# Kernel optimization log

Hardware: AMD Instinct MI355X
Metric: run time of the kernel (lower is better)

## Reference

```python
import jax, jax.numpy as jnp
import numpy as np

N, E, D, H, OUT = 100000, 1600000, 64, 64, 4


def _glorot(key, i, o):
    s = (6.0 / (i + o)) ** 0.5
    return jax.random.uniform(key, (i, o), jnp.float32, -s, s)


def setup_inputs() -> dict:
    key = jax.random.key(0)
    ks = jax.random.split(key, 5)
    x = jax.random.normal(ks[0], (N, D), jnp.float32)
    edge_index = jax.random.randint(ks[1], (2, E), 0, N, jnp.int32)
    return {
        "x": x,
        "edge_index": edge_index,
        "W0": _glorot(ks[2], D, H), "b0": jnp.zeros((H,), jnp.float32),
        "W1": _glorot(ks[3], H, H), "b1": jnp.zeros((H,), jnp.float32),
        "W2": _glorot(ks[4], H, OUT), "b2": jnp.zeros((OUT,), jnp.float32),
    }


def _gcn_layer(x, src, dst, W, b):
    # WeightedGCNConv.forward: remove_self_loops, then gcn_norm with
    # add_self_loops=True (self-loop weight 1), symmetric normalization,
    # scatter-add aggregation, then Linear.
    n = x.shape[0]
    w = (src != dst).astype(x.dtype)           # zero out original self loops
    deg = jax.ops.segment_sum(w, dst, num_segments=n) + 1.0  # +1 from added self loop
    dis = jax.lax.rsqrt(deg)                   # deg >= 1, no inf
    norm = dis[src] * w * dis[dst]             # [E]
    agg = jax.ops.segment_sum(norm[:, None] * x[src], dst, num_segments=n)
    agg = agg + (dis * dis)[:, None] * x       # self-loop contribution
    return agg @ W + b


def reference(x, edge_index, W0, b0, W1, b1, W2, b2):
    src, dst = edge_index[0], edge_index[1]    # flow source_to_target
    # Dropout is identity in eval mode.
    h = jax.nn.relu(_gcn_layer(x, src, dst, W0, b0))
    h = jax.nn.relu(_gcn_layer(h, src, dst, W1, b1))
    return _gcn_layer(h, src, dst, W2, b2)     # [N, 4]
```

## Files before the change

### kernel.cpp

```cpp
#include <hip/hip_runtime.h>
#include <hip/hip_fp16.h>


#define BLK 256
#define NBITS 7
#define NBW   (1 << NBITS)
#define G     8
#define CHUNK 4096
#define EPT   (CHUNK / BLK)
#define CAPG  384
#define PAD   16

__global__ void k_zero_i(int* __restrict__ p, int n) {
    int i = blockIdx.x * blockDim.x + threadIdx.x;
    if (i < n) p[i] = 0;
}

__global__ void k_binA(const int* __restrict__ src, const int* __restrict__ dst,
                       int* __restrict__ bcur, int* __restrict__ binned,
                       int E, int nb) {
    __shared__ int lcnt[1024];
    __shared__ int lbase[1024];
    int t = threadIdx.x;
    int g = blockIdx.x & (G - 1);
    for (int i = t; i < nb; i += BLK) lcnt[i] = 0;
    __syncthreads();

    int e0 = blockIdx.x * CHUNK;
    int bs[EPT], vs[EPT];
#pragma unroll
    for (int i = 0; i < EPT; ++i) {
        int e = e0 + i * BLK + t;
        bs[i] = -1;
        if (e < E) {
            int s = src[e], d = dst[e];
            if (s != d) {
                bs[i] = d >> NBITS;
                vs[i] = (s << NBITS) | (d & (NBW - 1));
                atomicAdd(&lcnt[bs[i]], 1);
            }
        }
    }
    __syncthreads();
    for (int i = t; i < nb; i += BLK) {
        int c = lcnt[i];
        lbase[i] = c ? atomicAdd(&bcur[(g * nb + i) * PAD], c) : 0;
    }
    __syncthreads();
    for (int i = t; i < nb; i += BLK) lcnt[i] = 0;
    __syncthreads();
#pragma unroll
    for (int i = 0; i < EPT; ++i) {
        if (bs[i] >= 0) {
            int p = lbase[bs[i]] + atomicAdd(&lcnt[bs[i]], 1);
            if (p < CAPG) binned[(size_t)(g * nb + bs[i]) * CAPG + p] = vs[i];
        }
    }
}

__global__ void k_bscan(const int* __restrict__ bcur, int* __restrict__ bbase, int nb) {
    __shared__ int sh[1024];
    int t = threadIdx.x;
    int v = 0;
    if (t < nb)
        for (int g = 0; g < G; ++g) v += min(bcur[(g * nb + t) * PAD], CAPG);
    sh[t] = v;
    __syncthreads();
    for (int off = 1; off < 1024; off <<= 1) {
        int u = (t >= off) ? sh[t - off] : 0;
        __syncthreads();
        sh[t] += u;
        __syncthreads();
    }
    if (t < nb) bbase[t] = sh[t] - v;
}

__global__ void k_binB(const int* __restrict__ bcur, const int* __restrict__ binned,
                       const int* __restrict__ bbase, int* __restrict__ rowstart,
                       float* __restrict__ dis, int* __restrict__ srcs,
                       int n, int nb) {
    __shared__ int cnt[NBW];
    __shared__ int scan[NBW];
    int b = blockIdx.x;
    int t = threadIdx.x;
    if (t < NBW) cnt[t] = 0;
    __syncthreads();
    for (int g = 0; g < G; ++g) {
        int m = min(bcur[(g * nb + b) * PAD], CAPG);
        const int* reg = binned + (size_t)(g * nb + b) * CAPG;
        for (int i = t; i < m; i += BLK)
            atomicAdd(&cnt[reg[i] & (NBW - 1)], 1);
    }
    __syncthreads();
    int c = 0;
    if (t < NBW) { c = cnt[t]; scan[t] = c; }
    __syncthreads();
    for (int off = 1; off < NBW; off <<= 1) {
        int u = (t < NBW && t >= off) ? scan[t - off] : 0;
        __syncthreads();
        if (t < NBW) scan[t] += u;
        __syncthreads();
    }
    int base = bbase[b];
    if (t < NBW) {
        int excl = scan[t] - c;
        int node = b * NBW + t;
        if (node < n) {
            rowstart[node] = base + excl;
            dis[node] = rsqrtf((float)c + 1.0f);
        }
        if (node == n) rowstart[n] = base + excl;
    }
    __syncthreads();
    if (t < NBW) scan[t] = scan[t] - c;
    __syncthreads();
    for (int g = 0; g < G; ++g) {
        int m = min(bcur[(g * nb + b) * PAD], CAPG);
        const int* reg = binned + (size_t)(g * nb + b) * CAPG;
        for (int i = t; i < m; i += BLK) {
            int v = reg[i];
            int p = atomicAdd(&scan[v & (NBW - 1)], 1);
            srcs[base + p] = v >> NBITS;
        }
    }
}

__device__ __forceinline__ float ldf(const float* p, long i) { return p[i]; }
__device__ __forceinline__ float ldf(const __half* p, long i) { return __half2float(p[i]); }

template <bool RELU, typename TIN>
__global__ void k_gemm64(const TIN* __restrict__ in, const float* __restrict__ W,
                         const float* __restrict__ dis, __half* __restrict__ z16, int n) {
    __shared__ float rows[4][64];
    int c  = threadIdx.x & 63;
    int r4 = threadIdx.x >> 6;
    float Wr[64];
#pragma unroll
    for (int k = 0; k < 64; ++k) Wr[k] = W[k * 64 + c];
    const float4* rp = reinterpret_cast<const float4*>(&rows[r4][0]);
    for (long base = (long)blockIdx.x * 4; base < n; base += (long)gridDim.x * 4) {
        long row = base + r4;
        __syncthreads();
        if (row < n) {
            float v = ldf(in, row * 64 + c);
            rows[r4][c] = RELU ? fmaxf(v, 0.0f) : v;
        }
        __syncthreads();
        if (row < n) {
            float acc = 0.0f;
#pragma unroll
            for (int k4 = 0; k4 < 16; ++k4) {
                float4 rv = rp[k4];
                acc = fmaf(rv.x, Wr[4 * k4 + 0], acc);
                acc = fmaf(rv.y, Wr[4 * k4 + 1], acc);
                acc = fmaf(rv.z, Wr[4 * k4 + 2], acc);
                acc = fmaf(rv.w, Wr[4 * k4 + 3], acc);
            }
            z16[row * 64 + c] = __float2half(dis[row] * acc);
        }
    }
}

__global__ void k_gemm4(const __half* __restrict__ in, const float* __restrict__ W,
                        const float* __restrict__ dis, float* __restrict__ z2, int n) {
    __shared__ float Wl[64 * 4];
    if (threadIdx.x < 64 * 4) Wl[threadIdx.x] = W[threadIdx.x];
    __syncthreads();
    long idx = (long)blockIdx.x * blockDim.x + threadIdx.x;
    long row = idx >> 2;
    int c    = (int)(idx & 3);
    if (row < n) {
        float acc = 0.0f;
#pragma unroll
        for (int k = 0; k < 64; ++k)
            acc = fmaf(fmaxf(__half2float(in[row * 64 + k]), 0.0f), Wl[k * 4 + c], acc);
        z2[idx] = dis[row] * acc;
    }
}

__global__ void k_aggregate(const __half2* __restrict__ z16, const int* __restrict__ rowstart,
                            const int* __restrict__ srcs, const float* __restrict__ dis,
                            const float* __restrict__ b, __half2* __restrict__ agg, int n) {
    int lane = threadIdx.x & 63;
    int node = blockIdx.x * (BLK / 64) + (threadIdx.x >> 6);
    if (node >= n) return;
    int p  = lane & 31;
    int hi = lane >> 5;
    float2 acc = make_float2(0.0f, 0.0f);
    if (hi == 0) {
        float2 v = __half22float2(z16[(long)node * 32 + p]);
        acc.x = v.x; acc.y = v.y;
    }
    int beg = rowstart[node], end = rowstart[node + 1];
    for (int base = beg; base < end; base += 64) {
        int rem = end - base;
        int m   = (rem < 64) ? rem : 64;
        int s   = (lane < m) ? srcs[base + lane] : 0;
        int me  = m & ~1;
#pragma unroll 8
        for (int j = 0; j < me; j += 2) {
            int sj = __shfl(s, j + hi);
            float2 v = __half22float2(z16[(long)sj * 32 + p]);
            acc.x += v.x; acc.y += v.y;
        }
        if (m & 1) {
            int sj = __shfl(s, m - 1);
            if (hi == 0) {
                float2 v = __half22float2(z16[(long)sj * 32 + p]);
                acc.x += v.x; acc.y += v.y;
            }
        }
    }
    acc.x += __shfl_xor(acc.x, 32);
    acc.y += __shfl_xor(acc.y, 32);
    if (hi == 0) {
        float dd = dis[node];
        agg[(long)node * 32 + p] =
            __floats2half2_rn(dd * acc.x + b[2 * p], dd * acc.y + b[2 * p + 1]);
    }
}

__global__ void k_agg4(const float* __restrict__ z2, const int* __restrict__ rowstart,
                       const int* __restrict__ srcs, const float* __restrict__ dis,
                       const float* __restrict__ b, float* __restrict__ out, int n) {
    long t = (long)blockIdx.x * blockDim.x + threadIdx.x;
    int i = (int)(t >> 2), c = (int)(t & 3);
    if (i < n) {
        float acc = z2[(long)i * 4 + c];
        int beg = rowstart[i], end = rowstart[i + 1];
        for (int e = beg; e < end; ++e)
            acc += z2[(long)srcs[e] * 4 + c];
        out[(long)i * 4 + c] = dis[i] * acc + b[c];
    }
}

extern "C" void kernel_launch(void* const* d_in, const int* in_sizes, int n_in,
                              void* d_out, int out_size, void* d_ws, size_t ws_size,
                              hipStream_t stream) {
    const float* x  = (const float*)d_in[0];
    const int*   ei = (const int*)d_in[1];
    const float* W0 = (const float*)d_in[2];
    const float* b0 = (const float*)d_in[3];
    const float* W1 = (const float*)d_in[4];
    const float* b1 = (const float*)d_in[5];
    const float* W2 = (const float*)d_in[6];
    const float* b2 = (const float*)d_in[7];
    float* out = (float*)d_out;

    const int n = in_sizes[0] / 64;
    const int E = in_sizes[1] / 2;
    const int* src = ei;
    const int* dst = ei + E;
    const int nb = (n + NBW - 1) / NBW;

    int*    bcur     = (int*)d_ws;
    int*    bbase    = bcur + G * nb * PAD;
    int*    rowstart = bbase + nb + 1;
    int*    srcs     = rowstart + n + 1;
    float*  dis      = (float*)(srcs + E);
    __half* z16      = (__half*)(dis + n);
    __half* bufA     = z16 + (size_t)n * 64;
    float*  y2       = (float*)(bufA + (size_t)n * 64);
    int*    binned   = (int*)bufA;

    const int gWave  = (n + (BLK / 64) - 1) / (BLK / 64);
    const int gN4    = (int)(((long)n * 4 + BLK - 1) / BLK);
    const int gGemm  = 2048;
    const int nchunk = (E + CHUNK - 1) / CHUNK;

    k_zero_i<<<(G * nb * PAD + BLK - 1) / BLK, BLK, 0, stream>>>(bcur, G * nb * PAD);
    k_binA<<<nchunk, BLK, 0, stream>>>(src, dst, bcur, binned, E, nb);
    k_bscan<<<1, 1024, 0, stream>>>(bcur, bbase, nb);
    k_binB<<<nb, BLK, 0, stream>>>(bcur, binned, bbase, rowstart, dis, srcs, n, nb);

    k_gemm64<false, float><<<gGemm, BLK, 0, stream>>>(x, W0, dis, z16, n);
    k_aggregate<<<gWave, BLK, 0, stream>>>((const __half2*)z16, rowstart, srcs, dis, b0,
                                           (__half2*)bufA, n);

    k_gemm64<true, __half><<<gGemm, BLK, 0, stream>>>(bufA, W1, dis, z16, n);
    k_aggregate<<<gWave, BLK, 0, stream>>>((const __half2*)z16, rowstart, srcs, dis, b1,
                                           (__half2*)bufA, n);

    k_gemm4<<<gN4, BLK, 0, stream>>>(bufA, W2, dis, y2, n);
    k_agg4<<<gN4, BLK, 0, stream>>>(y2, rowstart, srcs, dis, b2, out, n);
}
```

Measured before the change: 282.6 us.

## Fuse final 64x4 projection into second aggregation and widen gather to 8-byte loads

The aggregation kernel now has each lane load 4 halves (8 bytes) per neighbor, so a wave covers four neighbor rows per step instead of two, with a two-level shuffle reduction at the end. A templated variant applies bias, ReLU and the 64x4 W2 projection right after the layer-2 aggregation and writes only the 4-wide y2 row. This removes the separate k_gemm4 kernel and its write and read of the fp16 hidden buffer. In exchange it adds more shuffles per node, and the final projection now uses full-precision aggregated values instead of fp16-rounded ones.

```diff
diff --git a/kernel.cpp b/kernel.cpp
--- a/kernel.cpp
+++ b/kernel.cpp
@@ -161,62 +161,88 @@
     }
 }
 
-__global__ void k_gemm4(const __half* __restrict__ in, const float* __restrict__ W,
-                        const float* __restrict__ dis, float* __restrict__ z2, int n) {
-    __shared__ float Wl[64 * 4];
-    if (threadIdx.x < 64 * 4) Wl[threadIdx.x] = W[threadIdx.x];
-    __syncthreads();
-    long idx = (long)blockIdx.x * blockDim.x + threadIdx.x;
-    long row = idx >> 2;
-    int c    = (int)(idx & 3);
-    if (row < n) {
-        float acc = 0.0f;
-#pragma unroll
-        for (int k = 0; k < 64; ++k)
-            acc = fmaf(fmaxf(__half2float(in[row * 64 + k]), 0.0f), Wl[k * 4 + c], acc);
-        z2[idx] = dis[row] * acc;
-    }
-}
-
-__global__ void k_aggregate(const __half2* __restrict__ z16, const int* __restrict__ rowstart,
+template <bool FUSEW2>
+__global__ void k_aggregate(const float2* __restrict__ zrow, const int* __restrict__ rowstart,
                             const int* __restrict__ srcs, const float* __restrict__ dis,
-                            const float* __restrict__ b, __half2* __restrict__ agg, int n) {
+                            const float* __restrict__ bias, const float* __restrict__ W2,
+                            uint2* __restrict__ agg, float* __restrict__ y2, int n) {
+    __shared__ float W2l[64 * 4];
+    if constexpr (FUSEW2) {
+        if (threadIdx.x < 256) W2l[threadIdx.x] = W2[threadIdx.x];
+        __syncthreads();
+    }
     int lane = threadIdx.x & 63;
     int node = blockIdx.x * (BLK / 64) + (threadIdx.x >> 6);
     if (node >= n) return;
-    int p  = lane & 31;
-    int hi = lane >> 5;
-    float2 acc = make_float2(0.0f, 0.0f);
+    int p  = lane & 15;
+    int hi = lane >> 4;
+    float4 acc = make_float4(0.f, 0.f, 0.f, 0.f);
     if (hi == 0) {
-        float2 v = __half22float2(z16[(long)node * 32 + p]);
-        acc.x = v.x; acc.y = v.y;
+        float2 r = zrow[(long)node * 16 + p];
+        float2 a = __half22float2(*reinterpret_cast<__half2*>(&r.x));
+        float2 bq = __half22float2(*reinterpret_cast<__half2*>(&r.y));
+        acc = make_float4(a.x, a.y, bq.x, bq.y);
     }
     int beg = rowstart[node], end = rowstart[node + 1];
     for (int base = beg; base < end; base += 64) {
-        int rem = end - base;
-        int m   = (rem < 64) ? rem : 64;
-        int s   = (lane < m) ? srcs[base + lane] : 0;
-        int me  = m & ~1;
+        int m = min(end - base, 64);
+        int s = (lane < m) ? srcs[base + lane] : 0;
+        int mf = m & ~3;
 #pragma unroll 8
-        for (int j = 0; j < me; j += 2) {
+        for (int j = 0; j < mf; j += 4) {
             int sj = __shfl(s, j + hi);
-            float2 v = __half22float2(z16[(long)sj * 32 + p]);
-            acc.x += v.x; acc.y += v.y;
-        }
-        if (m & 1) {
-            int sj = __shfl(s, m - 1);
-            if (hi == 0) {
-                float2 v = __half22float2(z16[(long)sj * 32 + p]);
-                acc.x += v.x; acc.y += v.y;
+            float2 r = zrow[(long)sj * 16 + p];
+            float2 a = __half22float2(*reinterpret_cast<__half2*>(&r.x));
+            float2 bq = __half22float2(*reinterpret_cast<__half2*>(&r.y));
+            acc.x += a.x; acc.y += a.y; acc.z += bq.x; acc.w += bq.y;
+        }
+        if (m & 3) {
+            int idx = mf + hi;
+            int sj = __shfl(s, idx < 64 ? idx : 63);
+            if (idx < m) {
+                float2 r = zrow[(long)sj * 16 + p];
+                float2 a = __half22float2(*reinterpret_cast<__half2*>(&r.x));
+                float2 bq = __half22float2(*reinterpret_cast<__half2*>(&r.y));
+                acc.x += a.x; acc.y += a.y; acc.z += bq.x; acc.w += bq.y;
             }
         }
     }
-    acc.x += __shfl_xor(acc.x, 32);
-    acc.y += __shfl_xor(acc.y, 32);
-    if (hi == 0) {
-        float dd = dis[node];
-        agg[(long)node * 32 + p] =
-            __floats2half2_rn(dd * acc.x + b[2 * p], dd * acc.y + b[2 * p + 1]);
+    acc.x += __shfl_xor(acc.x, 16); acc.y += __shfl_xor(acc.y, 16);
+    acc.z += __shfl_xor(acc.z, 16); acc.w += __shfl_xor(acc.w, 16);
+    acc.x += __shfl_xor(acc.x, 32); acc.y += __shfl_xor(acc.y, 32);
+    acc.z += __shfl_xor(acc.z, 32); acc.w += __shfl_xor(acc.w, 32);
+
+    float dd = dis[node];
+    float4 bb = reinterpret_cast<const float4*>(bias)[p];
+    if constexpr (!FUSEW2) {
+        if (hi == 0) {
+            __half2 o0 = __floats2half2_rn(dd * acc.x + bb.x, dd * acc.y + bb.y);
+            __half2 o1 = __floats2half2_rn(dd * acc.z + bb.z, dd * acc.w + bb.w);
+            uint2 u;
+            u.x = *reinterpret_cast<unsigned int*>(&o0);
+            u.y = *reinterpret_cast<unsigned int*>(&o1);
+            agg[(long)node * 16 + p] = u;
+        }
+    } else {
+        float h0 = fmaxf(dd * acc.x + bb.x, 0.f);
+        float h1 = fmaxf(dd * acc.y + bb.y, 0.f);
+        float h2 = fmaxf(dd * acc.z + bb.z, 0.f);
+        float h3 = fmaxf(dd * acc.w + bb.w, 0.f);
+        float pc[4];
+#pragma unroll
+        for (int c = 0; c < 4; ++c) {
+            pc[c] = h0 * W2l[(4 * p + 0) * 4 + c] + h1 * W2l[(4 * p + 1) * 4 + c]
+                  + h2 * W2l[(4 * p + 2) * 4 + c] + h3 * W2l[(4 * p + 3) * 4 + c];
+        }
+#pragma unroll
+        for (int off = 1; off < 16; off <<= 1) {
+#pragma unroll
+            for (int c = 0; c < 4; ++c) pc[c] += __shfl_xor(pc[c], off);
+        }
+        if (lane == 0) {
+            reinterpret_cast<float4*>(y2)[node] =
+                make_float4(dd * pc[0], dd * pc[1], dd * pc[2], dd * pc[3]);
+        }
     }
 }
 
@@ -274,13 +300,12 @@
     k_binB<<<nb, BLK, 0, stream>>>(bcur, binned, bbase, rowstart, dis, srcs, n, nb);
 
     k_gemm64<false, float><<<gGemm, BLK, 0, stream>>>(x, W0, dis, z16, n);
-    k_aggregate<<<gWave, BLK, 0, stream>>>((const __half2*)z16, rowstart, srcs, dis, b0,
-                                           (__half2*)bufA, n);
+    k_aggregate<false><<<gWave, BLK, 0, stream>>>((const float2*)z16, rowstart, srcs, dis,
+                                                  b0, nullptr, (uint2*)bufA, nullptr, n);
 
     k_gemm64<true, __half><<<gGemm, BLK, 0, stream>>>(bufA, W1, dis, z16, n);
-    k_aggregate<<<gWave, BLK, 0, stream>>>((const __half2*)z16, rowstart, srcs, dis, b1,
-                                           (__half2*)bufA, n);
-
-    k_gemm4<<<gN4, BLK, 0, stream>>>(bufA, W2, dis, y2, n);
+    k_aggregate<true><<<gWave, BLK, 0, stream>>>((const float2*)z16, rowstart, srcs, dis,
+                                                 b1, W2, nullptr, y2, n);
+
     k_agg4<<<gN4, BLK, 0, stream>>>(y2, rowstart, srcs, dis, b2, out, n);
 }
```

Result: faster. 256.5 us (-9.3%).
